# Performance work log

Hardware: AMD Instinct MI355X
Metric: run time of the kernel (lower is better)

Reference implementation:

```python
import jax, jax.numpy as jnp
from jax import lax
import numpy as np

# init kwargs baked as constants (module hyperparameters)
T_LOW = 0.8
T_HIGH = 0.92
Z_RADIUS = 1
XY_RADIUS = 0
DUST_MIN_SIZE = 20


def _shifted(x, axis, step, fill):
    """Shift x by `step` along `axis`, filling vacated slots with `fill`."""
    pad = [(0, 0)] * x.ndim
    n = x.shape[axis]
    if step > 0:
        pad[axis] = (step, 0)
        xp = jnp.pad(x, pad, constant_values=fill)
        return lax.slice_in_dim(xp, 0, n, axis=axis)
    else:
        pad[axis] = (0, -step)
        xp = jnp.pad(x, pad, constant_values=fill)
        return lax.slice_in_dim(xp, -step, n - step, axis=axis)


def _dilate6(m):
    """Binary dilation with 6-connectivity (3D cross incl. center) on [B,D,H,W] bool."""
    out = m
    for ax in (1, 2, 3):
        out = out | _shifted(m, ax, 1, False) | _shifted(m, ax, -1, False)
    return out


def _neighbor_min6(l, big):
    """Min over 6-neighborhood (and self) of int labels; out-of-bounds = big."""
    out = l
    for ax in (1, 2, 3):
        out = jnp.minimum(out, jnp.minimum(_shifted(l, ax, 1, big), _shifted(l, ax, -1, big)))
    return out


def _postprocess(x):
    B, D, H, W = x.shape
    N = D * H * W

    # ---- hysteresis thresholding: grow strong seeds through weak mask ----
    weak = x >= T_LOW
    strong = x >= T_HIGH

    def h_cond(c):
        return c[1]

    def h_body(c):
        m, _ = c
        new = weak & _dilate6(m)
        return new, jnp.any(new != m)

    mask, _ = lax.while_loop(h_cond, h_body, (strong, jnp.array(True)))

    # ---- anisotropic closing: box SE (2*z_r+1, 2*xy_r+1, 2*xy_r+1) ----
    # dilation = max-pool (outside = background), erosion = min-pool (outside = foreground,
    # matching skimage's border_value=1 for erosion so borders are not eaten away)
    win = (1, 2 * Z_RADIUS + 1, 2 * XY_RADIUS + 1, 2 * XY_RADIUS + 1)
    ones = (1, 1, 1, 1)
    mf = mask.astype(jnp.float32)
    dil = lax.reduce_window(mf, -jnp.inf, lax.max, win, ones, 'SAME')
    ero = lax.reduce_window(dil, jnp.inf, lax.min, win, ones, 'SAME')
    mask = ero > 0.5

    # ---- remove_small_objects: CCL via min-label propagation (6-connectivity) ----
    big = jnp.int32(N)  # background sentinel
    flat_ids = jnp.arange(N, dtype=jnp.int32).reshape(1, D, H, W)
    init = jnp.where(mask, flat_ids, big)

    def c_cond(c):
        return c[1]

    def c_body(c):
        lab, _ = c
        new = jnp.where(mask, _neighbor_min6(lab, big), big)
        return new, jnp.any(new != lab)

    labels, _ = lax.while_loop(c_cond, c_body, (init, jnp.array(True)))

    labf = labels.reshape(B, N)
    wf = mask.reshape(B, N).astype(jnp.int32)
    counts = jax.vmap(lambda l, w: jax.ops.segment_sum(w, l, num_segments=N + 1))(labf, wf)
    sizes = jnp.take_along_axis(counts, labf, axis=1).reshape(B, D, H, W)
    keep = mask & (sizes >= DUST_MIN_SIZE)

    # original writes uint8 0/1 back into a float result tensor
    return keep.astype(jnp.float32)


def setup_inputs() -> dict:
    key = jax.random.key(0)
    outputs = jax.random.uniform(key, (8, 16, 384, 384), dtype=jnp.float32)
    return {"outputs": outputs}


def reference(outputs) -> jnp.ndarray:
    return _postprocess(outputs)
```

## Files before the change

kernel.cpp:

```cpp
#include <hip/hip_runtime.h>
#include <stdint.h>

#define B_ 8
#define D_ 16
#define H_ 384
#define W_ 384
constexpr int HW   = H_ * W_;
constexpr int DHW  = D_ * HW;
constexpr int NCOL = B_ * HW;
constexpr unsigned NRUN = (unsigned)NCOL * 8u;

constexpr float T_LOW  = 0.8f;
constexpr float T_HIGH = 0.92f;
constexpr unsigned DUST_MIN = 20u;
constexpr unsigned FLAGGED = 0xFFFFFFFEu;

constexpr int NBLK_QUAD = NCOL / 1024;

constexpr int PTW = 16, PTH = 16;
constexpr int PWB = W_ / PTW;
constexpr int PHB = H_ / PTH;
constexpr int NPATCH = B_ * PWB * PHB;
constexpr int NXCD = 8;
constexpr int CHUNK = NPATCH / NXCD;

constexpr int WPAIR_B = (PWB - 1) * H_;
constexpr int HPAIR_B = (PHB - 1) * W_;
constexpr int PAIR_B  = WPAIR_B + HPAIR_B;
constexpr int NPAIRS  = B_ * PAIR_B;

__device__ __forceinline__ unsigned gfind(unsigned* A, unsigned x) {
    for (;;) {
        unsigned p = A[x];
        if (p >= NRUN) return x;
        unsigned g = A[p];
        if (g >= NRUN) return p;
        A[x] = g;
        x = g;
    }
}

__device__ __forceinline__ unsigned groot_val(unsigned* A, unsigned x) {
    for (;;) {
        unsigned p = A[x];
        if (p >= NRUN) return p;
        unsigned g = A[p];
        if (g >= NRUN) return g;
        A[x] = g;
        x = g;
    }
}

__device__ __forceinline__ void set_flag(unsigned* A, unsigned x) {
    unsigned r = gfind(A, x);
    for (;;) {
        unsigned old = atomicMin(&A[r], FLAGGED);
        if (old >= NRUN) return;
        r = gfind(A, old);
    }
}

__device__ __forceinline__ void add_count(unsigned* A, unsigned x, unsigned cnt) {
    unsigned r = gfind(A, x);
    for (;;) {
        unsigned old = A[r];
        if (old < NRUN) { r = gfind(A, old); continue; }
        if (atomicCAS(&A[r], old, old - cnt) == old) return;
    }
}

__device__ __forceinline__ void gunite_flag(unsigned* A, unsigned a, unsigned b) {
    for (;;) {
        a = gfind(A, a);
        b = gfind(A, b);
        if (a == b) return;
        unsigned lo = a < b ? a : b;
        unsigned hi = a < b ? b : a;
        unsigned old = atomicMin(&A[hi], lo);
        if (old >= NRUN) {
            if (old == FLAGGED) set_flag(A, lo);
            return;
        }
        a = lo; b = old;
    }
}

__device__ __forceinline__ void gunite_cnt(unsigned* A, unsigned a, unsigned b) {
    for (;;) {
        a = gfind(A, a);
        b = gfind(A, b);
        if (a == b) return;
        unsigned lo = a < b ? a : b;
        unsigned hi = a < b ? b : a;
        unsigned old = atomicMin(&A[hi], lo);
        if (old >= NRUN) {
            unsigned cnt = 0xFFFFFFFFu - old;
            if (cnt) add_count(A, lo, cnt);
            return;
        }
        a = lo; b = old;
    }
}

__device__ __forceinline__ int runidx(unsigned m, int p) {
    unsigned starts = m & ~(m << 1);
    return __popc(starts & ((2u << p) - 1u)) - 1;
}

__device__ __forceinline__ int nruns(unsigned m) {
    return __popc(m & ~(m << 1));
}

__device__ __forceinline__ unsigned luf_find(unsigned* su, unsigned x) {
    for (;;) {
        unsigned p = su[x];
        if (p == x) return x;
        unsigned g = su[p];
        if (g == p) return p;
        su[x] = g;
        x = g;
    }
}

__device__ __forceinline__ void luf_union(unsigned* su, unsigned a, unsigned b) {
    for (;;) {
        a = luf_find(su, a);
        b = luf_find(su, b);
        if (a == b) return;
        unsigned lo = a < b ? a : b;
        unsigned hi = a < b ? b : a;
        unsigned old = atomicMin(&su[hi], lo);
        if (old == hi) return;
        a = lo; b = old;
    }
}

__device__ __forceinline__ void patch_unions(unsigned* su, const unsigned* sm,
                                             unsigned m, int t) {
    int lw = t & 15, lh = t >> 4;
    if (!m) return;
    if (lw < 15) {
        unsigned mB = sm[t + 1];
        unsigned ov = m & mB;
        while (ov) {
            int p = __ffs(ov) - 1;
            luf_union(su, (unsigned)runidx(m, p) * 256 + t,
                          (unsigned)runidx(mB, p) * 256 + t + 1);
            ov &= ov + (1u << p);
        }
    }
    if (lh < 15) {
        unsigned mB = sm[t + 16];
        unsigned ov = m & mB;
        while (ov) {
            int p = __ffs(ov) - 1;
            luf_union(su, (unsigned)runidx(m, p) * 256 + t,
                          (unsigned)runidx(mB, p) * 256 + t + 16);
            ov &= ov + (1u << p);
        }
    }
}

__device__ __forceinline__ int swz_blk(int d) {
    return (d % NXCD) * CHUNK + d / NXCD;
}


__global__ __launch_bounds__(256) void k_loc1(const float* __restrict__ x,
                                              unsigned short* __restrict__ weakm,
                                              unsigned* __restrict__ parent1) {
    __shared__ unsigned sm[256];
    __shared__ unsigned su[2048];
    __shared__ unsigned sf[2048];
    int blk = swz_blk(blockIdx.x);
    int b = blk / (PHB * PWB), pr = blk % (PHB * PWB);
    int h0 = (pr / PWB) * PTH, w0 = (pr % PWB) * PTW;
    int t = threadIdx.x;
    int c = b * HW + (h0 + (t >> 4)) * W_ + (w0 + (t & 15));
    const float* xp = x + (size_t)b * DHW + (size_t)(h0 + (t >> 4)) * W_ + (w0 + (t & 15));
    float vz[16];
    #pragma unroll
    for (int z = 0; z < 16; ++z) vz[z] = xp[(size_t)z * HW];
    unsigned m = 0, st = 0;
    #pragma unroll
    for (int z = 0; z < 16; ++z) {
        m  |= (vz[z] >= T_LOW  ? 1u : 0u) << z;
        st |= (vz[z] >= T_HIGH ? 1u : 0u) << z;
    }
    weakm[c] = (unsigned short)m;
    sm[t] = m;
    #pragma unroll
    for (int i = 0; i < 8; ++i) { su[i * 256 + t] = i * 256 + t; sf[i * 256 + t] = 0; }
    __syncthreads();
    patch_unions(su, sm, m, t);
    __syncthreads();
    if (st) {
        unsigned ov = st;
        while (ov) {
            int p = __ffs(ov) - 1;
            sf[luf_find(su, (unsigned)runidx(m, p) * 256 + t)] = 1u;
            ov &= ov + (1u << p);
        }
    }
    __syncthreads();
    int nr = nruns(m);
    for (int i = 0; i < nr; ++i) {
        unsigned lid = (unsigned)i * 256 + t;
        unsigned lr  = luf_find(su, lid);
        unsigned gid = (unsigned)i * NCOL + c;
        if (lr == lid) parent1[gid] = sf[lid] ? FLAGGED : 0xFFFFFFFFu;
        else {
            unsigned tt = lr & 255u, ss = lr >> 8;
            parent1[gid] = ss * NCOL +
                (unsigned)(b * HW + (h0 + (int)(tt >> 4)) * W_ + (w0 + (int)(tt & 15)));
        }
    }
}

__global__ __launch_bounds__(256) void k_bnd1(const unsigned short* __restrict__ weakm,
                                              unsigned* parent1) {
    int e = blockIdx.x * 256 + threadIdx.x;
    if (e >= NPAIRS) return;
    int b = e / PAIR_B, r = e % PAIR_B;
    int cA, cB;
    if (r < WPAIR_B) {
        int h = r / (PWB - 1), wi = r % (PWB - 1);
        cA = b * HW + h * W_ + wi * PTW + (PTW - 1);
        cB = cA + 1;
    } else {
        r -= WPAIR_B;
        int hi = r / W_, w = r % W_;
        cA = b * HW + (hi * PTH + (PTH - 1)) * W_ + w;
        cB = cA + W_;
    }
    unsigned mA = weakm[cA];
    unsigned mB = weakm[cB];
    unsigned ov = mA & mB;
    while (ov) {
        int p = __ffs(ov) - 1;
        gunite_flag(parent1, (unsigned)runidx(mA, p) * NCOL + cA,
                             (unsigned)runidx(mB, p) * NCOL + cB);
        ov &= ov + (1u << p);
    }
}

__global__ __launch_bounds__(256) void k_loc2(const unsigned short* __restrict__ weakm,
                                              unsigned* parent1,
                                              unsigned short* __restrict__ closed,
                                              unsigned* __restrict__ parent2) {
    __shared__ unsigned sm[256];
    __shared__ unsigned su[2048];
    __shared__ unsigned sc[2048];
    int blk = swz_blk(blockIdx.x);
    int b = blk / (PHB * PWB), pr = blk % (PHB * PWB);
    int h0 = (pr / PWB) * PTH, w0 = (pr % PWB) * PTW;
    int t = threadIdx.x;
    int c = b * HW + (h0 + (t >> 4)) * W_ + (w0 + (t & 15));
    unsigned wk = weakm[c];
    int nrw = nruns(wk);
    unsigned pv[6];
    #pragma unroll
    for (int i = 0; i < 6; ++i) if (i < nrw) pv[i] = parent1[(unsigned)i * NCOL + c];
    unsigned m = 0;
    {
        unsigned rem = wk; int idx = 0;
        while (rem) {
            int p = __ffs(rem) - 1;
            unsigned tt = rem >> p;
            int len = __ffs(~tt) - 1;
            unsigned runmask = ((1u << len) - 1u) << p;
            unsigned rv;
            if (idx < 6) { unsigned v = pv[idx]; rv = (v >= NRUN) ? v : groot_val(parent1, v); }
            else rv = groot_val(parent1, (unsigned)idx * NCOL + c);
            if (rv == FLAGGED) m |= runmask;
            rem &= ~runmask; ++idx;
        }
    }
    unsigned dil = (m | (m << 1) | (m >> 1)) & 0xFFFFu;
    unsigned ero = dil & ((dil << 1) | 1u) & ((dil >> 1) | 0x8000u);
    closed[c] = (unsigned short)ero;

    sm[t] = ero;
    #pragma unroll
    for (int i = 0; i < 8; ++i) { su[i * 256 + t] = i * 256 + t; sc[i * 256 + t] = 0; }
    __syncthreads();
    patch_unions(su, sm, ero, t);
    __syncthreads();
    {
        unsigned rem = ero; int idx = 0;
        while (rem) {
            int p = __ffs(rem) - 1;
            unsigned tt = rem >> p;
            int len = __ffs(~tt) - 1;
            unsigned runmask = ((1u << len) - 1u) << p;
            atomicAdd(&sc[luf_find(su, (unsigned)idx * 256 + t)], (unsigned)len);
            rem &= ~runmask; ++idx;
        }
    }
    __syncthreads();
    int nr = nruns(ero);
    for (int i = 0; i < nr; ++i) {
        unsigned lid = (unsigned)i * 256 + t;
        unsigned lr  = luf_find(su, lid);
        unsigned gid = (unsigned)i * NCOL + c;
        if (lr == lid) parent2[gid] = 0xFFFFFFFFu - sc[lid];
        else {
            unsigned tt = lr & 255u, ss = lr >> 8;
            parent2[gid] = ss * NCOL +
                (unsigned)(b * HW + (h0 + (int)(tt >> 4)) * W_ + (w0 + (int)(tt & 15)));
        }
    }
}

__global__ __launch_bounds__(256) void k_bnd2(const unsigned short* __restrict__ closed,
                                              unsigned* parent2) {
    int e = blockIdx.x * 256 + threadIdx.x;
    if (e >= NPAIRS) return;
    int b = e / PAIR_B, r = e % PAIR_B;
    int cA, cB;
    if (r < WPAIR_B) {
        int h = r / (PWB - 1), wi = r % (PWB - 1);
        cA = b * HW + h * W_ + wi * PTW + (PTW - 1);
        cB = cA + 1;
    } else {
        r -= WPAIR_B;
        int hi = r / W_, w = r % W_;
        cA = b * HW + (hi * PTH + (PTH - 1)) * W_ + w;
        cB = cA + W_;
    }
    unsigned mA = closed[cA];
    unsigned mB = closed[cB];
    unsigned ov = mA & mB;
    while (ov) {
        int p = __ffs(ov) - 1;
        gunite_cnt(parent2, (unsigned)runidx(mA, p) * NCOL + cA,
                            (unsigned)runidx(mB, p) * NCOL + cB);
        ov &= ov + (1u << p);
    }
}

__global__ __launch_bounds__(256) void k_out(const unsigned short* __restrict__ closed,
                                             unsigned* parent2,
                                             float* __restrict__ out) {
    int q = blockIdx.x * 256 + threadIdx.x;
    int c0 = q * 4;
    int b = c0 / HW, off = c0 - b * HW;
    ushort4 cc4 = *(const ushort4*)(closed + c0);
    unsigned fg[4] = {cc4.x, cc4.y, cc4.z, cc4.w};
    unsigned pv[4][6];
    int nr[4];
    #pragma unroll
    for (int j = 0; j < 4; ++j) {
        nr[j] = nruns(fg[j]);
        #pragma unroll
        for (int i = 0; i < 6; ++i)
            if (i < nr[j]) pv[j][i] = parent2[(unsigned)i * NCOL + (c0 + j)];
    }
    unsigned keep[4];
    #pragma unroll
    for (int j = 0; j < 4; ++j) {
        int c = c0 + j;
        unsigned k = 0;
        unsigned rem = fg[j]; int idx = 0;
        while (rem) {
            int p = __ffs(rem) - 1;
            unsigned tt = rem >> p;
            int len = __ffs(~tt) - 1;
            unsigned runmask = ((1u << len) - 1u) << p;
            unsigned rv;
            if (idx < 6) { unsigned v = pv[j][idx]; rv = (v >= NRUN) ? v : groot_val(parent2, v); }
            else rv = groot_val(parent2, (unsigned)idx * NCOL + c);
            if (0xFFFFFFFFu - rv >= DUST_MIN) k |= runmask;
            rem &= ~runmask; ++idx;
        }
        keep[j] = k;
    }
    float* op = out + (size_t)b * DHW + off;
    #pragma unroll
    for (int z = 0; z < D_; ++z) {
        *(float4*)(op + (size_t)z * HW) =
            make_float4((keep[0] >> z) & 1u ? 1.0f : 0.0f,
                        (keep[1] >> z) & 1u ? 1.0f : 0.0f,
                        (keep[2] >> z) & 1u ? 1.0f : 0.0f,
                        (keep[3] >> z) & 1u ? 1.0f : 0.0f);
    }
}

extern "C" void kernel_launch(void* const* d_in, const int* in_sizes, int n_in,
                              void* d_out, int out_size, void* d_ws, size_t ws_size,
                              hipStream_t stream) {
    const float* x = (const float*)d_in[0];
    float* out = (float*)d_out;

    const size_t sz_parent = (size_t)NRUN * 4;
    const size_t sz_mask   = (size_t)NCOL * 2;
    if (ws_size < 2 * sz_parent + 2 * sz_mask) return;
    char* ws = (char*)d_ws;
    unsigned*       parent1 = (unsigned*)ws;
    unsigned*       parent2 = (unsigned*)(ws + sz_parent);
    unsigned short* weakm   = (unsigned short*)(ws + 2 * sz_parent);
    unsigned short* closed  = (unsigned short*)(ws + 2 * sz_parent + sz_mask);

    dim3 blk(256);
    dim3 grdL(NPATCH), grdB((NPAIRS + 255) / 256), grdQ(NBLK_QUAD);

    k_loc1<<<grdL, blk, 0, stream>>>(x, weakm, parent1);
    k_bnd1<<<grdB, blk, 0, stream>>>(weakm, parent1);

    k_loc2<<<grdL, blk, 0, stream>>>(weakm, parent1, closed, parent2);
    k_bnd2<<<grdB, blk, 0, stream>>>(closed, parent2);
    k_out<<<grdQ, blk, 0, stream>>>(closed, parent2, out);
}
```

Before: 251.9 us.

## Enlarge local union-find patches to 32x32 with four columns per thread

Local connected-component patches grow from 16x16 to 32x32 columns. Each of the 256 threads now handles four columns, and shared union-find arrays are resized to match (the flag array shrinks to bytes). This is meant to cut the number of cross-patch boundary pairs, and with it the global union work and atomics in the boundary kernels. In exchange, shared-memory use per block rises sharply, which lowers occupancy, and in-patch union-find chains get longer.

After: 315.3 us. 25.2% more time.

```diff
diff --git a/kernel.cpp b/kernel.cpp
--- a/kernel.cpp
+++ b/kernel.cpp
@@ -17,7 +17,7 @@
 
 constexpr int NBLK_QUAD = NCOL / 1024;
 
-constexpr int PTW = 16, PTH = 16;
+constexpr int PTW = 32, PTH = 32;
 constexpr int PWB = W_ / PTW;
 constexpr int PHB = H_ / PTH;
 constexpr int NPATCH = B_ * PWB * PHB;
@@ -135,27 +135,26 @@
     }
 }
 
-__device__ __forceinline__ void patch_unions(unsigned* su, const unsigned* sm,
-                                             unsigned m, int t) {
-    int lw = t & 15, lh = t >> 4;
+__device__ __forceinline__ void punions32(unsigned* su, const unsigned* sm,
+                                          unsigned m, int lc, bool rok, bool dok) {
     if (!m) return;
-    if (lw < 15) {
-        unsigned mB = sm[t + 1];
+    if (rok) {
+        unsigned mB = sm[lc + 1];
         unsigned ov = m & mB;
         while (ov) {
             int p = __ffs(ov) - 1;
-            luf_union(su, (unsigned)runidx(m, p) * 256 + t,
-                          (unsigned)runidx(mB, p) * 256 + t + 1);
+            luf_union(su, (unsigned)runidx(m, p) * 1024 + lc,
+                          (unsigned)runidx(mB, p) * 1024 + lc + 1);
             ov &= ov + (1u << p);
         }
     }
-    if (lh < 15) {
-        unsigned mB = sm[t + 16];
+    if (dok) {
+        unsigned mB = sm[lc + 32];
         unsigned ov = m & mB;
         while (ov) {
             int p = __ffs(ov) - 1;
-            luf_union(su, (unsigned)runidx(m, p) * 256 + t,
-                          (unsigned)runidx(mB, p) * 256 + t + 16);
+            luf_union(su, (unsigned)runidx(m, p) * 1024 + lc,
+                          (unsigned)runidx(mB, p) * 1024 + lc + 32);
             ov &= ov + (1u << p);
         }
     }
@@ -169,50 +168,71 @@
 __global__ __launch_bounds__(256) void k_loc1(const float* __restrict__ x,
                                               unsigned short* __restrict__ weakm,
                                               unsigned* __restrict__ parent1) {
-    __shared__ unsigned sm[256];
-    __shared__ unsigned su[2048];
-    __shared__ unsigned sf[2048];
+    __shared__ unsigned sm[1024];
+    __shared__ unsigned su[8192];
+    __shared__ unsigned char sf[8192];
     int blk = swz_blk(blockIdx.x);
     int b = blk / (PHB * PWB), pr = blk % (PHB * PWB);
     int h0 = (pr / PWB) * PTH, w0 = (pr % PWB) * PTW;
     int t = threadIdx.x;
-    int c = b * HW + (h0 + (t >> 4)) * W_ + (w0 + (t & 15));
-    const float* xp = x + (size_t)b * DHW + (size_t)(h0 + (t >> 4)) * W_ + (w0 + (t & 15));
-    float vz[16];
-    #pragma unroll
-    for (int z = 0; z < 16; ++z) vz[z] = xp[(size_t)z * HW];
-    unsigned m = 0, st = 0;
-    #pragma unroll
-    for (int z = 0; z < 16; ++z) {
-        m  |= (vz[z] >= T_LOW  ? 1u : 0u) << z;
-        st |= (vz[z] >= T_HIGH ? 1u : 0u) << z;
-    }
-    weakm[c] = (unsigned short)m;
-    sm[t] = m;
-    #pragma unroll
-    for (int i = 0; i < 8; ++i) { su[i * 256 + t] = i * 256 + t; sf[i * 256 + t] = 0; }
-    __syncthreads();
-    patch_unions(su, sm, m, t);
-    __syncthreads();
-    if (st) {
-        unsigned ov = st;
+    int lw = t & 31, lh = t >> 5;
+    unsigned m[4], st[4];
+    #pragma unroll
+    for (int k = 0; k < 4; ++k) {
+        int r = lh + 8 * k;
+        const float* xp = x + (size_t)b * DHW + (size_t)(h0 + r) * W_ + (w0 + lw);
+        float vz[16];
+        #pragma unroll
+        for (int z = 0; z < 16; ++z) vz[z] = xp[(size_t)z * HW];
+        unsigned mm = 0, ss = 0;
+        #pragma unroll
+        for (int z = 0; z < 16; ++z) {
+            mm |= (vz[z] >= T_LOW  ? 1u : 0u) << z;
+            ss |= (vz[z] >= T_HIGH ? 1u : 0u) << z;
+        }
+        m[k] = mm; st[k] = ss;
+        weakm[b * HW + (h0 + r) * W_ + (w0 + lw)] = (unsigned short)mm;
+        sm[r * 32 + lw] = mm;
+    }
+    #pragma unroll
+    for (int i = 0; i < 32; ++i) su[i * 256 + t] = i * 256 + t;
+    unsigned* sf32 = (unsigned*)sf;
+    #pragma unroll
+    for (int i = 0; i < 8; ++i) sf32[i * 256 + t] = 0;
+    __syncthreads();
+    #pragma unroll
+    for (int k = 0; k < 4; ++k) {
+        int r = lh + 8 * k, lc = r * 32 + lw;
+        punions32(su, sm, m[k], lc, lw < 31, r < 31);
+    }
+    __syncthreads();
+    #pragma unroll
+    for (int k = 0; k < 4; ++k) {
+        unsigned ov = st[k];
+        if (!ov) continue;
+        int lc = (lh + 8 * k) * 32 + lw;
         while (ov) {
             int p = __ffs(ov) - 1;
-            sf[luf_find(su, (unsigned)runidx(m, p) * 256 + t)] = 1u;
+            sf[luf_find(su, (unsigned)runidx(m[k], p) * 1024 + lc)] = 1;
             ov &= ov + (1u << p);
         }
     }
     __syncthreads();
-    int nr = nruns(m);
-    for (int i = 0; i < nr; ++i) {
-        unsigned lid = (unsigned)i * 256 + t;
-        unsigned lr  = luf_find(su, lid);
-        unsigned gid = (unsigned)i * NCOL + c;
-        if (lr == lid) parent1[gid] = sf[lid] ? FLAGGED : 0xFFFFFFFFu;
-        else {
-            unsigned tt = lr & 255u, ss = lr >> 8;
-            parent1[gid] = ss * NCOL +
-                (unsigned)(b * HW + (h0 + (int)(tt >> 4)) * W_ + (w0 + (int)(tt & 15)));
+    #pragma unroll
+    for (int k = 0; k < 4; ++k) {
+        int r = lh + 8 * k, lc = r * 32 + lw;
+        int c = b * HW + (h0 + r) * W_ + (w0 + lw);
+        int nr = nruns(m[k]);
+        for (int i = 0; i < nr; ++i) {
+            unsigned lid = (unsigned)i * 1024 + lc;
+            unsigned lr  = luf_find(su, lid);
+            unsigned gid = (unsigned)i * NCOL + c;
+            if (lr == lid) parent1[gid] = sf[lid] ? FLAGGED : 0xFFFFFFFFu;
+            else {
+                unsigned tt = lr & 1023u, ss2 = lr >> 10;
+                parent1[gid] = ss2 * NCOL +
+                    (unsigned)(b * HW + (h0 + (int)(tt >> 5)) * W_ + (w0 + (int)(tt & 31)));
+            }
         }
     }
 }
@@ -248,66 +268,92 @@
                                               unsigned* parent1,
                                               unsigned short* __restrict__ closed,
                                               unsigned* __restrict__ parent2) {
-    __shared__ unsigned sm[256];
-    __shared__ unsigned su[2048];
-    __shared__ unsigned sc[2048];
+    __shared__ unsigned sm[1024];
+    __shared__ unsigned su[6144];
+    __shared__ unsigned sc[6144];
     int blk = swz_blk(blockIdx.x);
     int b = blk / (PHB * PWB), pr = blk % (PHB * PWB);
     int h0 = (pr / PWB) * PTH, w0 = (pr % PWB) * PTW;
     int t = threadIdx.x;
-    int c = b * HW + (h0 + (t >> 4)) * W_ + (w0 + (t & 15));
-    unsigned wk = weakm[c];
-    int nrw = nruns(wk);
-    unsigned pv[6];
-    #pragma unroll
-    for (int i = 0; i < 6; ++i) if (i < nrw) pv[i] = parent1[(unsigned)i * NCOL + c];
-    unsigned m = 0;
-    {
-        unsigned rem = wk; int idx = 0;
+    int lw = t & 31, lh = t >> 5;
+    unsigned wk[4];
+    int c_[4];
+    #pragma unroll
+    for (int k = 0; k < 4; ++k) {
+        int r = lh + 8 * k;
+        c_[k] = b * HW + (h0 + r) * W_ + (w0 + lw);
+        wk[k] = weakm[c_[k]];
+    }
+    unsigned pv[4][6];
+    #pragma unroll
+    for (int k = 0; k < 4; ++k) {
+        int nrw = nruns(wk[k]);
+        #pragma unroll
+        for (int i = 0; i < 6; ++i)
+            if (i < nrw) pv[k][i] = parent1[(unsigned)i * NCOL + c_[k]];
+    }
+    unsigned ero[4];
+    #pragma unroll
+    for (int k = 0; k < 4; ++k) {
+        unsigned m = 0;
+        unsigned rem = wk[k]; int idx = 0;
         while (rem) {
             int p = __ffs(rem) - 1;
             unsigned tt = rem >> p;
             int len = __ffs(~tt) - 1;
             unsigned runmask = ((1u << len) - 1u) << p;
             unsigned rv;
-            if (idx < 6) { unsigned v = pv[idx]; rv = (v >= NRUN) ? v : groot_val(parent1, v); }
-            else rv = groot_val(parent1, (unsigned)idx * NCOL + c);
+            if (idx < 6) { unsigned v = pv[k][idx]; rv = (v >= NRUN) ? v : groot_val(parent1, v); }
+            else rv = groot_val(parent1, (unsigned)idx * NCOL + c_[k]);
             if (rv == FLAGGED) m |= runmask;
             rem &= ~runmask; ++idx;
         }
-    }
-    unsigned dil = (m | (m << 1) | (m >> 1)) & 0xFFFFu;
-    unsigned ero = dil & ((dil << 1) | 1u) & ((dil >> 1) | 0x8000u);
-    closed[c] = (unsigned short)ero;
-
-    sm[t] = ero;
-    #pragma unroll
-    for (int i = 0; i < 8; ++i) { su[i * 256 + t] = i * 256 + t; sc[i * 256 + t] = 0; }
-    __syncthreads();
-    patch_unions(su, sm, ero, t);
-    __syncthreads();
-    {
-        unsigned rem = ero; int idx = 0;
+        unsigned dil = (m | (m << 1) | (m >> 1)) & 0xFFFFu;
+        unsigned e = dil & ((dil << 1) | 1u) & ((dil >> 1) | 0x8000u);
+        ero[k] = e;
+        closed[c_[k]] = (unsigned short)e;
+        sm[(lh + 8 * k) * 32 + lw] = e;
+    }
+    #pragma unroll
+    for (int i = 0; i < 24; ++i) su[i * 256 + t] = i * 256 + t;
+    #pragma unroll
+    for (int i = 0; i < 24; ++i) sc[i * 256 + t] = 0;
+    __syncthreads();
+    #pragma unroll
+    for (int k = 0; k < 4; ++k) {
+        int r = lh + 8 * k, lc = r * 32 + lw;
+        punions32(su, sm, ero[k], lc, lw < 31, r < 31);
+    }
+    __syncthreads();
+    #pragma unroll
+    for (int k = 0; k < 4; ++k) {
+        int lc = (lh + 8 * k) * 32 + lw;
+        unsigned rem = ero[k]; int idx = 0;
         while (rem) {
             int p = __ffs(rem) - 1;
             unsigned tt = rem >> p;
             int len = __ffs(~tt) - 1;
             unsigned runmask = ((1u << len) - 1u) << p;
-            atomicAdd(&sc[luf_find(su, (unsigned)idx * 256 + t)], (unsigned)len);
+            atomicAdd(&sc[luf_find(su, (unsigned)idx * 1024 + lc)], (unsigned)len);
             rem &= ~runmask; ++idx;
         }
     }
     __syncthreads();
-    int nr = nruns(ero);
-    for (int i = 0; i < nr; ++i) {
-        unsigned lid = (unsigned)i * 256 + t;
-        unsigned lr  = luf_find(su, lid);
-        unsigned gid = (unsigned)i * NCOL + c;
-        if (lr == lid) parent2[gid] = 0xFFFFFFFFu - sc[lid];
-        else {
-            unsigned tt = lr & 255u, ss = lr >> 8;
-            parent2[gid] = ss * NCOL +
-                (unsigned)(b * HW + (h0 + (int)(tt >> 4)) * W_ + (w0 + (int)(tt & 15)));
+    #pragma unroll
+    for (int k = 0; k < 4; ++k) {
+        int r = lh + 8 * k, lc = r * 32 + lw;
+        int c = c_[k];
+        int nr = nruns(ero[k]);
+        for (int i = 0; i < nr; ++i) {
+            unsigned lid = (unsigned)i * 1024 + lc;
+            unsigned lr  = luf_find(su, lid);
+            unsigned gid = (unsigned)i * NCOL + c;
+            if (lr == lid) parent2[gid] = 0xFFFFFFFFu - sc[lid];
+            else {
+                unsigned tt = lr & 1023u, ss2 = lr >> 10;
+                parent2[gid] = ss2 * NCOL +
+                    (unsigned)(b * HW + (h0 + (int)(tt >> 5)) * W_ + (w0 + (int)(tt & 31)));
+            }
         }
     }
 }
```
